# Kernel tuning notes

Hardware: AMD Instinct MI355X
Metric: run time of the kernel (lower is better)

The kernel has to match this reference:

```python
import jax, jax.numpy as jnp
import numpy as np

E, L, R, H, V = 8, 8, 4, 4096, 32000
B, S = 2, 1024


def setup_inputs() -> dict:
    key = jax.random.key(0)
    ks = jax.random.split(key, 8)
    scale = 0.02
    return {
        "hidden_state": jax.random.normal(ks[0], (B, S, H), jnp.float32),
        "router_w": jax.random.normal(ks[1], (E, H), jnp.float32) * scale,
        "router_b": jnp.zeros((E,), jnp.float32),
        "expert_B": jax.random.normal(ks[2], (E, L, R, H), jnp.float32) * scale,
        "expert_A": jax.random.normal(ks[3], (E, L, H, R), jnp.float32) * scale,
        "deep_B": jax.random.normal(ks[4], (L, R, H), jnp.float32) * scale,
        "deep_A": jax.random.normal(ks[5], (L, H, R), jnp.float32) * scale,
        "lm_head_w": jax.random.normal(ks[6], (V, H), jnp.float32) * scale,
    }


def reference(hidden_state, router_w, router_b, expert_B, expert_A,
              deep_B, deep_A, lm_head_w):
    h = hidden_state  # [B,S,H]
    # Router applies softmax internally; forward softmaxes AGAIN (faithful to source).
    router_logits = jax.nn.softmax(
        jnp.einsum('bsh,eh->bse', h, router_w) + router_b, axis=-1)
    router_probs = jax.nn.softmax(router_logits, axis=-1)  # [B,S,E]
    psum = jnp.sum(router_probs, axis=-1, keepdims=True)   # [B,S,1] (== 1)

    n_layers = deep_B.shape[0]
    for i in range(n_layers):
        # All experts' LoRA low-rank projections in one batched contraction.
        z = jnp.einsum('bsh,erh->bser', h, expert_B[:, i])  # [B,S,E,r]
        # combined = sum_e p_e * (h + z_e @ A_e^T) = h * sum_e p_e + weighted delta
        zw = z * router_probs[..., None]                    # [B,S,E,r]
        delta = jnp.einsum('bser,ehr->bsh', zw, expert_A[:, i])
        combined = h * psum + delta                         # [B,S,H]
        # Residual deep LoRA merge: x + (x @ B^T) @ A^T
        low = jnp.einsum('bsh,rh->bsr', combined, deep_B[i])
        h = combined + jnp.einsum('bsr,hr->bsh', low, deep_A[i])

    lm_logits = jnp.einsum('bsh,vh->bsv', h, lm_head_w)  # [B,S,V]
    return (lm_logits, router_logits)
```

## Files before the change

### kernel.cpp

```cpp
#include <hip/hip_runtime.h>
#include <cstdint>
#include <cstddef>

#define HD 4096
#define EE 8
#define LL 8
#define RR 4
#define VV 32000
#define NTOK 2048
#define NKT (HD / 64)
#define T8 8

typedef __attribute__((ext_vector_type(8))) short bf16x8;
typedef __attribute__((ext_vector_type(4))) float f32x4;

static __device__ __forceinline__ unsigned short f2bf(float f) {
    unsigned int u = __builtin_bit_cast(unsigned int, f);
    unsigned int r = (u + 0x7FFFu + ((u >> 16) & 1u)) >> 16;
    return (unsigned short)r;
}

__global__ __launch_bounds__(512, 2) void fused_layers(
    const float* __restrict__ h_in,
    const float* __restrict__ router_w,
    const float* __restrict__ router_b,
    const float* __restrict__ expert_B,
    const float* __restrict__ expert_A,
    const float* __restrict__ deep_B,
    const float* __restrict__ deep_A,
    float* __restrict__ router_logits,
    unsigned short* __restrict__ h_out)
{
    __shared__ float h_lds[T8][HD];
    __shared__ float zw_lds[T8][32];
    __shared__ float probs_lds[T8][EE];
    __shared__ float psum_lds[T8];
    __shared__ float red[8][T8][4];
    __shared__ float low_lds[T8][4];

    const int tid  = threadIdx.x;
    const int lane = tid & 63;
    const int wv   = tid >> 6;
    const int t0   = blockIdx.x * T8;

    for (int t = 0; t < T8; ++t) {
        const float4* src = (const float4*)(h_in + (size_t)(t0 + t) * HD);
        float4* dst = (float4*)h_lds[t];
        #pragma unroll
        for (int q = 0; q < 2; ++q) dst[tid + q * 512] = src[tid + q * 512];
    }
    __syncthreads();

    {
        float racc[EE];
        #pragma unroll
        for (int e = 0; e < EE; ++e) racc[e] = 0.f;
        const float4* h4 = (const float4*)h_lds[wv];
        for (int k4 = 0; k4 < HD / 256; ++k4) {
            int idx = lane + k4 * 64;
            float4 hv = h4[idx];
            #pragma unroll
            for (int e = 0; e < EE; ++e) {
                float4 w4 = ((const float4*)(router_w + e * HD))[idx];
                racc[e] += w4.x * hv.x + w4.y * hv.y + w4.z * hv.z + w4.w * hv.w;
            }
        }
        #pragma unroll
        for (int e = 0; e < EE; ++e)
            for (int m = 1; m < 64; m <<= 1) racc[e] += __shfl_xor(racc[e], m);
        if (lane == 0) {
            float lg[EE], mx = -1e30f;
            #pragma unroll
            for (int e = 0; e < EE; ++e) { lg[e] = racc[e] + router_b[e]; mx = fmaxf(mx, lg[e]); }
            float s = 0.f;
            #pragma unroll
            for (int e = 0; e < EE; ++e) { lg[e] = expf(lg[e] - mx); s += lg[e]; }
            float inv = 1.f / s;
            float p1[EE], mx2 = -1e30f;
            #pragma unroll
            for (int e = 0; e < EE; ++e) { p1[e] = lg[e] * inv; mx2 = fmaxf(mx2, p1[e]); }
            float s2 = 0.f, q2[EE];
            #pragma unroll
            for (int e = 0; e < EE; ++e) { q2[e] = expf(p1[e] - mx2); s2 += q2[e]; }
            float inv2 = 1.f / s2, ps = 0.f;
            #pragma unroll
            for (int e = 0; e < EE; ++e) {
                float p2 = q2[e] * inv2;
                probs_lds[wv][e] = p2;
                ps += p2;
                router_logits[(size_t)(t0 + wv) * EE + e] = p1[e];
            }
            psum_lds[wv] = ps;
        }
    }
    __syncthreads();

    for (int li = 0; li < LL; ++li) {
        {
            float zacc[4][T8] = {};
            const float4* bp4[4];
            #pragma unroll
            for (int j = 0; j < 4; ++j) {
                int er = wv * 4 + j;
                int e = er >> 2, r = er & 3;
                bp4[j] = (const float4*)(expert_B + (size_t)((e * LL + li) * RR + r) * HD);
            }
            for (int k4 = 0; k4 < HD / 256; ++k4) {
                int idx = lane + k4 * 64;
                float4 hv[T8];
                #pragma unroll
                for (int t = 0; t < T8; ++t) hv[t] = ((const float4*)h_lds[t])[idx];
                #pragma unroll
                for (int j = 0; j < 4; ++j) {
                    float4 w4 = bp4[j][idx];
                    #pragma unroll
                    for (int t = 0; t < T8; ++t)
                        zacc[j][t] += w4.x * hv[t].x + w4.y * hv[t].y +
                                      w4.z * hv[t].z + w4.w * hv[t].w;
                }
            }
            #pragma unroll
            for (int j = 0; j < 4; ++j)
                #pragma unroll
                for (int t = 0; t < T8; ++t) {
                    float v = zacc[j][t];
                    for (int m = 1; m < 64; m <<= 1) v += __shfl_xor(v, m);
                    zacc[j][t] = v;
                }
            if (lane == 0) {
                #pragma unroll
                for (int j = 0; j < 4; ++j) {
                    int er = wv * 4 + j;
                    #pragma unroll
                    for (int t = 0; t < T8; ++t)
                        zw_lds[t][er] = zacc[j][t] * probs_lds[t][er >> 2];
                }
            }
        }
        __syncthreads();

        float dacc[T8][8] = {};
        const int pbase = wv * 512 + lane;
        for (int e = 0; e < EE; ++e) {
            float zwt[T8][4];
            #pragma unroll
            for (int t = 0; t < T8; ++t)
                #pragma unroll
                for (int r = 0; r < RR; ++r) zwt[t][r] = zw_lds[t][e * 4 + r];
            const float4* ap = (const float4*)expert_A + (size_t)(e * LL + li) * HD;
            #pragma unroll
            for (int it = 0; it < 8; ++it) {
                float4 a4 = ap[pbase + it * 64];
                #pragma unroll
                for (int t = 0; t < T8; ++t)
                    dacc[t][it] += zwt[t][0] * a4.x + zwt[t][1] * a4.y +
                                   zwt[t][2] * a4.z + zwt[t][3] * a4.w;
            }
        }

        float lowacc[T8][4] = {};
        float psv[T8];
        #pragma unroll
        for (int t = 0; t < T8; ++t) psv[t] = psum_lds[t];
        const float* dbp = deep_B + (size_t)li * (RR * HD);
        #pragma unroll
        for (int it = 0; it < 8; ++it) {
            int pos = pbase + it * 64;
            float db0 = dbp[pos], db1 = dbp[HD + pos], db2 = dbp[2 * HD + pos], db3 = dbp[3 * HD + pos];
            #pragma unroll
            for (int t = 0; t < T8; ++t) {
                float c = h_lds[t][pos] * psv[t] + dacc[t][it];
                h_lds[t][pos] = c;
                lowacc[t][0] += c * db0; lowacc[t][1] += c * db1;
                lowacc[t][2] += c * db2; lowacc[t][3] += c * db3;
            }
        }
        #pragma unroll
        for (int t = 0; t < T8; ++t)
            #pragma unroll
            for (int r = 0; r < RR; ++r) {
                float v = lowacc[t][r];
                for (int m = 1; m < 64; m <<= 1) v += __shfl_xor(v, m);
                lowacc[t][r] = v;
            }
        if (lane == 0) {
            #pragma unroll
            for (int t = 0; t < T8; ++t)
                #pragma unroll
                for (int r = 0; r < RR; ++r) red[wv][t][r] = lowacc[t][r];
        }
        __syncthreads();
        if (tid < 32) {
            int t = tid >> 2, r = tid & 3;
            float s = 0.f;
            #pragma unroll
            for (int w = 0; w < 8; ++w) s += red[w][t][r];
            low_lds[t][r] = s;
        }
        __syncthreads();

        {
            float lw[T8][4];
            #pragma unroll
            for (int t = 0; t < T8; ++t)
                #pragma unroll
                for (int r = 0; r < RR; ++r) lw[t][r] = low_lds[t][r];
            const float4* dap = (const float4*)deep_A + (size_t)li * HD;
            #pragma unroll
            for (int it = 0; it < 8; ++it) {
                int pos = pbase + it * 64;
                float4 a4 = dap[pos];
                #pragma unroll
                for (int t = 0; t < T8; ++t)
                    h_lds[t][pos] += lw[t][0] * a4.x + lw[t][1] * a4.y +
                                     lw[t][2] * a4.z + lw[t][3] * a4.w;
            }
        }
        __syncthreads();
    }

    for (int t = 0; t < T8; ++t) {
        ushort4* dst = (ushort4*)(h_out + (size_t)(t0 + t) * HD);
        const float4* src = (const float4*)h_lds[t];
        #pragma unroll
        for (int q = 0; q < 2; ++q) {
            int c = tid + q * 512;
            float4 v = src[c];
            ushort4 o;
            o.x = f2bf(v.x); o.y = f2bf(v.y); o.z = f2bf(v.z); o.w = f2bf(v.w);
            dst[c] = o;
        }
    }
}

__global__ __launch_bounds__(256) void cvt_kernel(const float4* __restrict__ in,
                                                  ushort4* __restrict__ out, int n4)
{
    int i = blockIdx.x * 256 + threadIdx.x;
    int stride = gridDim.x * 256;
    for (; i < n4; i += stride) {
        float4 v = in[i];
        ushort4 o;
        o.x = f2bf(v.x); o.y = f2bf(v.y); o.z = f2bf(v.z); o.w = f2bf(v.w);
        out[i] = o;
    }
}

#define GLD(src, dst) __builtin_amdgcn_global_load_lds( \
    (const __attribute__((address_space(1))) unsigned int*)(src), \
    (__attribute__((address_space(3))) unsigned int*)(dst), 16, 0, 0)

#define STAGE(pp, matoff, bufv, hh, ktv) do { \
    char* db_ = smem + (bufv) * 65536 + (matoff) + (hh) * 16384 + wv * 1024; \
    GLD(pp[0] + (size_t)(hh) * (128ull * HD * 2) + (size_t)(ktv) * 128, db_); \
    GLD(pp[1] + (size_t)(hh) * (128ull * HD * 2) + (size_t)(ktv) * 128, db_ + 8192); \
} while (0)

#define LDSREAD(off) (*(const bf16x8*)(smem + (off)))

__global__ __launch_bounds__(512, 2) void lm_gemm256(
    const unsigned short* __restrict__ A,
    const unsigned short* __restrict__ Bw,
    float* __restrict__ C)
{
    __shared__ __attribute__((aligned(128))) char smem[131072];

    const int bid = blockIdx.x;
    const int swz = (bid & 7) * 125 + (bid >> 3);
    const int bm = swz & 7;
    const int bn = swz >> 3;

    const int tid  = threadIdx.x;
    const int lane = tid & 63;
    const int wv   = tid >> 6;
    const int wr   = wv >> 2;
    const int wc   = wv & 3;

    const char* pA[2];
    const char* pB[2];
    #pragma unroll
    for (int q = 0; q < 2; ++q) {
        int off = (q * 512 + tid) * 16;
        int p = off ^ (((off >> 9) & 1) << 5);
        int st = p >> 10;
        int r  = (st >> 1) * 16 + ((p >> 6) & 15);
        int cb = (st & 1) * 64 + (p & 63);
        pA[q] = (const char*)(A  + (size_t)(bm * 256 + r) * HD) + cb;
        pB[q] = (const char*)(Bw + (size_t)(bn * 256 + r) * HD) + cb;
    }

    const int xlane = ((lane >> 3) & 1) << 5;
    const int abase = ((wr * 8) << 11) + ((lane & 15) << 6) + ((lane >> 4) << 4);
    const int bbase = 32768 + ((wc * 4) << 11) + ((lane & 15) << 6) + ((lane >> 4) << 4);

    f32x4 acc[8][4] = {};
    bf16x8 aF[4][2], bF0[2][2][2], bF1[2][2];

    STAGE(pB, 32768, 0, 0, 0);
    STAGE(pB, 32768, 0, 1, 0);
    STAGE(pA, 0,     0, 0, 0);
    STAGE(pA, 0,     0, 1, 0);
    STAGE(pB, 32768, 1, 0, 1);
    STAGE(pB, 32768, 1, 1, 1);
    asm volatile("s_waitcnt vmcnt(4)" ::: "memory");
    __builtin_amdgcn_s_barrier();
    __builtin_amdgcn_sched_barrier(0);
    #pragma unroll
    for (int n = 0; n < 2; ++n)
        #pragma unroll
        for (int ks = 0; ks < 2; ++ks)
            bF0[0][n][ks] = LDSREAD(((bbase + (n << 11) + (ks << 10)) ^ xlane));

    #pragma unroll 2
    for (int kt = 0; kt < NKT; ++kt) {
        const int cur = kt & 1;
        const int oth = cur ^ 1;
        const int cb0 = cur << 16;

        #pragma unroll
        for (int i = 0; i < 4; ++i)
            #pragma unroll
            for (int ks = 0; ks < 2; ++ks)
                aF[i][ks] = LDSREAD(cb0 + ((abase + (i << 11) + (ks << 10)) ^ xlane));
        if (kt + 1 < NKT) STAGE(pA, 0, oth, 0, kt + 1);
        __builtin_amdgcn_s_barrier();
        __builtin_amdgcn_sched_barrier(0);
        __builtin_amdgcn_s_setprio(1);
        #pragma unroll
        for (int ks = 0; ks < 2; ++ks)
            #pragma unroll
            for (int i = 0; i < 4; ++i)
                #pragma unroll
                for (int n = 0; n < 2; ++n)
                    acc[i][n] = __builtin_amdgcn_mfma_f32_16x16x32_bf16(
                        aF[i][ks], bF0[cur][n][ks], acc[i][n], 0, 0, 0);
        __builtin_amdgcn_s_setprio(0);
        __builtin_amdgcn_s_barrier();
        __builtin_amdgcn_sched_barrier(0);

        #pragma unroll
        for (int n = 0; n < 2; ++n)
            #pragma unroll
            for (int ks = 0; ks < 2; ++ks)
                bF1[n][ks] = LDSREAD(cb0 + ((bbase + ((n + 2) << 11) + (ks << 10)) ^ xlane));
        if (kt + 1 < NKT) STAGE(pA, 0, oth, 1, kt + 1);
        __builtin_amdgcn_s_barrier();
        __builtin_amdgcn_sched_barrier(0);
        __builtin_amdgcn_s_setprio(1);
        #pragma unroll
        for (int ks = 0; ks < 2; ++ks)
            #pragma unroll
            for (int i = 0; i < 4; ++i)
                #pragma unroll
                for (int n = 0; n < 2; ++n)
                    acc[i][n + 2] = __builtin_amdgcn_mfma_f32_16x16x32_bf16(
                        aF[i][ks], bF1[n][ks], acc[i][n + 2], 0, 0, 0);
        __builtin_amdgcn_s_setprio(0);
        __builtin_amdgcn_s_barrier();
        __builtin_amdgcn_sched_barrier(0);

        #pragma unroll
        for (int i = 0; i < 4; ++i)
            #pragma unroll
            for (int ks = 0; ks < 2; ++ks)
                aF[i][ks] = LDSREAD(cb0 + ((abase + ((i + 4) << 11) + (ks << 10)) ^ xlane));
        if (kt + 2 < NKT) STAGE(pB, 32768, cur, 0, kt + 2);
        __builtin_amdgcn_s_barrier();
        __builtin_amdgcn_sched_barrier(0);
        __builtin_amdgcn_s_setprio(1);
        #pragma unroll
        for (int ks = 0; ks < 2; ++ks)
            #pragma unroll
            for (int i = 0; i < 4; ++i)
                #pragma unroll
                for (int n = 0; n < 2; ++n)
                    acc[i + 4][n + 2] = __builtin_amdgcn_mfma_f32_16x16x32_bf16(
                        aF[i][ks], bF1[n][ks], acc[i + 4][n + 2], 0, 0, 0);
        __builtin_amdgcn_s_setprio(0);
        __builtin_amdgcn_s_barrier();
        __builtin_amdgcn_sched_barrier(0);

        if (kt + 2 < NKT) {
            STAGE(pB, 32768, cur, 1, kt + 2);
            asm volatile("s_waitcnt vmcnt(4)" ::: "memory");
        } else {
            asm volatile("s_waitcnt vmcnt(0)" ::: "memory");
        }
        __builtin_amdgcn_s_barrier();
        __builtin_amdgcn_sched_barrier(0);
        if (kt + 1 < NKT) {
            const int nb0 = oth << 16;
            #pragma unroll
            for (int n = 0; n < 2; ++n)
                #pragma unroll
                for (int ks = 0; ks < 2; ++ks)
                    bF0[oth][n][ks] = LDSREAD(nb0 + ((bbase + (n << 11) + (ks << 10)) ^ xlane));
        }
        __builtin_amdgcn_s_setprio(1);
        #pragma unroll
        for (int ks = 0; ks < 2; ++ks)
            #pragma unroll
            for (int i = 0; i < 4; ++i)
                #pragma unroll
                for (int n = 0; n < 2; ++n)
                    acc[i + 4][n] = __builtin_amdgcn_mfma_f32_16x16x32_bf16(
                        aF[i][ks], bF0[cur][n][ks], acc[i + 4][n], 0, 0, 0);
        __builtin_amdgcn_s_setprio(0);
        __builtin_amdgcn_s_barrier();
        __builtin_amdgcn_sched_barrier(0);
    }

    const int crow0 = bm * 256 + wr * 128 + ((lane >> 4) << 2);
    const int ccol0 = bn * 256 + wc * 64 + (lane & 15);
    #pragma unroll
    for (int fm = 0; fm < 8; ++fm)
        #pragma unroll
        for (int fn = 0; fn < 4; ++fn) {
            int row = crow0 + fm * 16;
            int col = ccol0 + fn * 16;
            #pragma unroll
            for (int j = 0; j < 4; ++j)
                C[(size_t)(row + j) * VV + col] = acc[fm][fn][j];
        }
}

extern "C" void kernel_launch(void* const* d_in, const int* in_sizes, int n_in,
                              void* d_out, int out_size, void* d_ws, size_t ws_size,
                              hipStream_t stream) {
    const float* h_in      = (const float*)d_in[0];
    const float* router_w  = (const float*)d_in[1];
    const float* router_b  = (const float*)d_in[2];
    const float* expert_B  = (const float*)d_in[3];
    const float* expert_A  = (const float*)d_in[4];
    const float* deep_B    = (const float*)d_in[5];
    const float* deep_A    = (const float*)d_in[6];
    const float* lm_head_w = (const float*)d_in[7];

    float* out = (float*)d_out;
    float* router_logits_out = out + (size_t)NTOK * VV;

    unsigned short* h_bf = (unsigned short*)d_ws;
    unsigned short* w_bf = (unsigned short*)((char*)d_ws + (size_t)NTOK * HD * 2);

    fused_layers<<<dim3(NTOK / T8), dim3(512), 0, stream>>>(
        h_in, router_w, router_b, expert_B, expert_A, deep_B, deep_A,
        router_logits_out, h_bf);

    cvt_kernel<<<dim3(4096), dim3(256), 0, stream>>>(
        (const float4*)lm_head_w, (ushort4*)w_bf, VV * HD / 4);

    lm_gemm256<<<dim3((NTOK / 256) * (VV / 256)), dim3(512), 0, stream>>>(
        h_bf, w_bf, out);
}
```

Measured before the change: 964.4 us.

## Fuse lm_head fp32-to-bf16 conversion into GEMM B-tile staging

Removes the standalone weight conversion kernel and has the LM-head GEMM load fp32 weight tiles into registers, pack them to bf16, and write them to LDS. This avoids writing and rereading a bf16 copy of the weight every call. In exchange, B tiles are fetched as fp32 (twice the bytes) by every block sharing them, and the B path moves from async global-to-LDS loads to register staging with extra VGPRs and conversion ALU work in the main loop.

```diff
diff --git a/kernel.cpp b/kernel.cpp
--- a/kernel.cpp
+++ b/kernel.cpp
@@ -18,6 +18,15 @@
     unsigned int u = __builtin_bit_cast(unsigned int, f);
     unsigned int r = (u + 0x7FFFu + ((u >> 16) & 1u)) >> 16;
     return (unsigned short)r;
+}
+
+static __device__ __forceinline__ int4 pack_bf16_8(float4 lo, float4 hi) {
+    int4 r;
+    r.x = (int)((unsigned)f2bf(lo.x) | ((unsigned)f2bf(lo.y) << 16));
+    r.y = (int)((unsigned)f2bf(lo.z) | ((unsigned)f2bf(lo.w) << 16));
+    r.z = (int)((unsigned)f2bf(hi.x) | ((unsigned)f2bf(hi.y) << 16));
+    r.w = (int)((unsigned)f2bf(hi.z) | ((unsigned)f2bf(hi.w) << 16));
+    return r;
 }
 
 __global__ __launch_bounds__(512, 2) void fused_layers(
@@ -233,34 +242,36 @@
     }
 }
 
-__global__ __launch_bounds__(256) void cvt_kernel(const float4* __restrict__ in,
-                                                  ushort4* __restrict__ out, int n4)
-{
-    int i = blockIdx.x * 256 + threadIdx.x;
-    int stride = gridDim.x * 256;
-    for (; i < n4; i += stride) {
-        float4 v = in[i];
-        ushort4 o;
-        o.x = f2bf(v.x); o.y = f2bf(v.y); o.z = f2bf(v.z); o.w = f2bf(v.w);
-        out[i] = o;
-    }
-}
-
 #define GLD(src, dst) __builtin_amdgcn_global_load_lds( \
     (const __attribute__((address_space(1))) unsigned int*)(src), \
     (__attribute__((address_space(3))) unsigned int*)(dst), 16, 0, 0)
 
-#define STAGE(pp, matoff, bufv, hh, ktv) do { \
-    char* db_ = smem + (bufv) * 65536 + (matoff) + (hh) * 16384 + wv * 1024; \
-    GLD(pp[0] + (size_t)(hh) * (128ull * HD * 2) + (size_t)(ktv) * 128, db_); \
-    GLD(pp[1] + (size_t)(hh) * (128ull * HD * 2) + (size_t)(ktv) * 128, db_ + 8192); \
+#define STAGE_A(bufv, hh, ktv) do { \
+    char* da_ = smem + (bufv) * 65536 + (hh) * 16384 + wv * 1024; \
+    GLD(pA[0] + (size_t)(hh) * (128ull * HD * 2) + (size_t)(ktv) * 128, da_); \
+    GLD(pA[1] + (size_t)(hh) * (128ull * HD * 2) + (size_t)(ktv) * 128, da_ + 8192); \
+} while (0)
+
+#define LB_LOAD(hh, ktv, d0, d1, d2, d3) do { \
+    const char* s0_ = pB32[0] + (size_t)(hh) * 2097152ull + (size_t)(ktv) * 256; \
+    const char* s1_ = pB32[1] + (size_t)(hh) * 2097152ull + (size_t)(ktv) * 256; \
+    d0 = *(const float4*)(s0_);      d1 = *(const float4*)(s0_ + 16); \
+    d2 = *(const float4*)(s1_);      d3 = *(const float4*)(s1_ + 16); \
+} while (0)
+
+#define B_WRITE(bufv, hh, d0, d1, d2, d3) do { \
+    int4 w0_ = pack_bf16_8(d0, d1); \
+    int4 w1_ = pack_bf16_8(d2, d3); \
+    char* bb_ = smem + (bufv) * 65536 + 32768 + (hh) * 16384 + tid * 16; \
+    *(int4*)(bb_)        = w0_; \
+    *(int4*)(bb_ + 8192) = w1_; \
 } while (0)
 
 #define LDSREAD(off) (*(const bf16x8*)(smem + (off)))
 
 __global__ __launch_bounds__(512, 2) void lm_gemm256(
     const unsigned short* __restrict__ A,
-    const unsigned short* __restrict__ Bw,
+    const float* __restrict__ Bw32,
     float* __restrict__ C)
 {
     __shared__ __attribute__((aligned(128))) char smem[131072];
@@ -277,7 +288,7 @@
     const int wc   = wv & 3;
 
     const char* pA[2];
-    const char* pB[2];
+    const char* pB32[2];
     #pragma unroll
     for (int q = 0; q < 2; ++q) {
         int off = (q * 512 + tid) * 16;
@@ -285,8 +296,8 @@
         int st = p >> 10;
         int r  = (st >> 1) * 16 + ((p >> 6) & 15);
         int cb = (st & 1) * 64 + (p & 63);
-        pA[q] = (const char*)(A  + (size_t)(bm * 256 + r) * HD) + cb;
-        pB[q] = (const char*)(Bw + (size_t)(bn * 256 + r) * HD) + cb;
+        pA[q]   = (const char*)(A + (size_t)(bm * 256 + r) * HD) + cb;
+        pB32[q] = (const char*)Bw32 + (size_t)(bn * 256 + r) * HD * 4 + cb * 2;
     }
 
     const int xlane = ((lane >> 3) & 1) << 5;
@@ -294,22 +305,22 @@
     const int bbase = 32768 + ((wc * 4) << 11) + ((lane & 15) << 6) + ((lane >> 4) << 4);
 
     f32x4 acc[8][4] = {};
-    bf16x8 aF[4][2], bF0[2][2][2], bF1[2][2];
-
-    STAGE(pB, 32768, 0, 0, 0);
-    STAGE(pB, 32768, 0, 1, 0);
-    STAGE(pA, 0,     0, 0, 0);
-    STAGE(pA, 0,     0, 1, 0);
-    STAGE(pB, 32768, 1, 0, 1);
-    STAGE(pB, 32768, 1, 1, 1);
-    asm volatile("s_waitcnt vmcnt(4)" ::: "memory");
+    bf16x8 aF[4][2], bF0[2][2], bF1[2][2];
+    float4 rb0, rb1, rb2, rb3, rc0, rc1, rc2, rc3;
+
+    LB_LOAD(0, 0, rb0, rb1, rb2, rb3);
+    LB_LOAD(1, 0, rc0, rc1, rc2, rc3);
+    STAGE_A(0, 0, 0);
+    STAGE_A(0, 1, 0);
+    B_WRITE(0, 0, rb0, rb1, rb2, rb3);
+    B_WRITE(0, 1, rc0, rc1, rc2, rc3);
+    LB_LOAD(0, 1, rb0, rb1, rb2, rb3);
+    LB_LOAD(1, 1, rc0, rc1, rc2, rc3);
+    B_WRITE(1, 0, rb0, rb1, rb2, rb3);
+    B_WRITE(1, 1, rc0, rc1, rc2, rc3);
+    asm volatile("s_waitcnt vmcnt(0) lgkmcnt(0)" ::: "memory");
     __builtin_amdgcn_s_barrier();
     __builtin_amdgcn_sched_barrier(0);
-    #pragma unroll
-    for (int n = 0; n < 2; ++n)
-        #pragma unroll
-        for (int ks = 0; ks < 2; ++ks)
-            bF0[0][n][ks] = LDSREAD(((bbase + (n << 11) + (ks << 10)) ^ xlane));
 
     #pragma unroll 2
     for (int kt = 0; kt < NKT; ++kt) {
@@ -322,7 +333,17 @@
             #pragma unroll
             for (int ks = 0; ks < 2; ++ks)
                 aF[i][ks] = LDSREAD(cb0 + ((abase + (i << 11) + (ks << 10)) ^ xlane));
-        if (kt + 1 < NKT) STAGE(pA, 0, oth, 0, kt + 1);
+        #pragma unroll
+        for (int n = 0; n < 2; ++n)
+            #pragma unroll
+            for (int ks = 0; ks < 2; ++ks)
+                bF0[n][ks] = LDSREAD(cb0 + ((bbase + (n << 11) + (ks << 10)) ^ xlane));
+        if (kt + 1 < NKT) {
+            STAGE_A(oth, 0, kt + 1);
+            STAGE_A(oth, 1, kt + 1);
+        }
+        __builtin_amdgcn_sched_barrier(0);
+        if (kt + 2 < NKT) LB_LOAD(0, kt + 2, rb0, rb1, rb2, rb3);
         __builtin_amdgcn_s_barrier();
         __builtin_amdgcn_sched_barrier(0);
         __builtin_amdgcn_s_setprio(1);
@@ -333,7 +354,7 @@
                 #pragma unroll
                 for (int n = 0; n < 2; ++n)
                     acc[i][n] = __builtin_amdgcn_mfma_f32_16x16x32_bf16(
-                        aF[i][ks], bF0[cur][n][ks], acc[i][n], 0, 0, 0);
+                        aF[i][ks], bF0[n][ks], acc[i][n], 0, 0, 0);
         __builtin_amdgcn_s_setprio(0);
         __builtin_amdgcn_s_barrier();
         __builtin_amdgcn_sched_barrier(0);
@@ -343,7 +364,7 @@
             #pragma unroll
             for (int ks = 0; ks < 2; ++ks)
                 bF1[n][ks] = LDSREAD(cb0 + ((bbase + ((n + 2) << 11) + (ks << 10)) ^ xlane));
-        if (kt + 1 < NKT) STAGE(pA, 0, oth, 1, kt + 1);
+        if (kt + 2 < NKT) LB_LOAD(1, kt + 2, rc0, rc1, rc2, rc3);
         __builtin_amdgcn_s_barrier();
         __builtin_amdgcn_sched_barrier(0);
         __builtin_amdgcn_s_setprio(1);
@@ -364,7 +385,7 @@
             #pragma unroll
             for (int ks = 0; ks < 2; ++ks)
                 aF[i][ks] = LDSREAD(cb0 + ((abase + ((i + 4) << 11) + (ks << 10)) ^ xlane));
-        if (kt + 2 < NKT) STAGE(pB, 32768, cur, 0, kt + 2);
+        if (kt + 2 < NKT) B_WRITE(cur, 0, rb0, rb1, rb2, rb3);
         __builtin_amdgcn_s_barrier();
         __builtin_amdgcn_sched_barrier(0);
         __builtin_amdgcn_s_setprio(1);
@@ -380,22 +401,13 @@
         __builtin_amdgcn_s_barrier();
         __builtin_amdgcn_sched_barrier(0);
 
-        if (kt + 2 < NKT) {
-            STAGE(pB, 32768, cur, 1, kt + 2);
-            asm volatile("s_waitcnt vmcnt(4)" ::: "memory");
-        } else {
-            asm volatile("s_waitcnt vmcnt(0)" ::: "memory");
-        }
-        __builtin_amdgcn_s_barrier();
-        __builtin_amdgcn_sched_barrier(0);
-        if (kt + 1 < NKT) {
-            const int nb0 = oth << 16;
-            #pragma unroll
-            for (int n = 0; n < 2; ++n)
-                #pragma unroll
-                for (int ks = 0; ks < 2; ++ks)
-                    bF0[oth][n][ks] = LDSREAD(nb0 + ((bbase + (n << 11) + (ks << 10)) ^ xlane));
-        }
+        if (kt + 2 < NKT) B_WRITE(cur, 1, rc0, rc1, rc2, rc3);
+        if (kt >= NKT - 2)
+            asm volatile("s_waitcnt vmcnt(0) lgkmcnt(0)" ::: "memory");
+        else
+            asm volatile("s_waitcnt lgkmcnt(0)" ::: "memory");
+        __builtin_amdgcn_s_barrier();
+        __builtin_amdgcn_sched_barrier(0);
         __builtin_amdgcn_s_setprio(1);
         #pragma unroll
         for (int ks = 0; ks < 2; ++ks)
@@ -404,7 +416,7 @@
                 #pragma unroll
                 for (int n = 0; n < 2; ++n)
                     acc[i + 4][n] = __builtin_amdgcn_mfma_f32_16x16x32_bf16(
-                        aF[i][ks], bF0[cur][n][ks], acc[i + 4][n], 0, 0, 0);
+                        aF[i][ks], bF0[n][ks], acc[i + 4][n], 0, 0, 0);
         __builtin_amdgcn_s_setprio(0);
         __builtin_amdgcn_s_barrier();
         __builtin_amdgcn_sched_barrier(0);
@@ -440,15 +452,11 @@
     float* router_logits_out = out + (size_t)NTOK * VV;
 
     unsigned short* h_bf = (unsigned short*)d_ws;
-    unsigned short* w_bf = (unsigned short*)((char*)d_ws + (size_t)NTOK * HD * 2);
 
     fused_layers<<<dim3(NTOK / T8), dim3(512), 0, stream>>>(
         h_in, router_w, router_b, expert_B, expert_A, deep_B, deep_A,
         router_logits_out, h_bf);
 
-    cvt_kernel<<<dim3(4096), dim3(256), 0, stream>>>(
-        (const float4*)lm_head_w, (ushort4*)w_bf, VV * HD / 4);
-
     lm_gemm256<<<dim3((NTOK / 256) * (VV / 256)), dim3(512), 0, stream>>>(
-        h_bf, w_bf, out);
+        h_bf, lm_head_w, out);
 }
```

Result: slower. 3.706 ms (+284.3%).
